# Optimization experiments

Measured on AMD Instinct MI355X. Metric: run time of the kernel, lower is better.

The kernel has to match this reference:

```python
import jax, jax.numpy as jnp
import numpy as np

INPUT_DIM = 1024
EMBED_DIM = 1024
NUM_HEADS = 16
HEAD_DIM = EMBED_DIM // NUM_HEADS


def _xavier_uniform(key, shape):
    fan_in, fan_out = shape[1], shape[0]
    limit = float(np.sqrt(6.0 / (fan_in + fan_out)))
    return jax.random.uniform(key, shape, jnp.float32, -limit, limit)


def setup_inputs() -> dict:
    key = jax.random.key(0)
    kx, kqkv, ko = jax.random.split(key, 3)
    x = jax.random.normal(kx, (2, 2048, INPUT_DIM), jnp.float32)
    # torch Linear stores weight as [out, in]; we keep that convention
    w_qkv = _xavier_uniform(kqkv, (3 * EMBED_DIM, INPUT_DIM))
    b_qkv = jnp.zeros((3 * EMBED_DIM,), jnp.float32)
    w_o = _xavier_uniform(ko, (EMBED_DIM, EMBED_DIM))
    b_o = jnp.zeros((EMBED_DIM,), jnp.float32)
    return {"x": x, "w_qkv": w_qkv, "b_qkv": b_qkv, "w_o": w_o, "b_o": b_o}


def reference(x, w_qkv, b_qkv, w_o, b_o):
    B, S, _ = x.shape
    H, D = NUM_HEADS, HEAD_DIM
    qkv = jnp.einsum("bsi,oi->bso", x, w_qkv) + b_qkv          # [B,S,3E]
    qkv = qkv.reshape(B, S, H, 3 * D).transpose(0, 2, 1, 3)    # [B,H,S,3D]
    q, k, v = jnp.split(qkv, 3, axis=-1)                        # each [B,H,S,D]
    scores = jnp.einsum("bhqd,bhkd->bhqk", q, k) / jnp.sqrt(jnp.float32(D))
    attn = jax.nn.softmax(scores, axis=-1)                      # [B,H,S,S]
    vals = jnp.einsum("bhqk,bhkd->bhqd", attn, v)               # [B,H,S,D]
    vals = vals.transpose(0, 2, 1, 3).reshape(B, S, H * D)      # [B,S,E]
    return jnp.einsum("bse,oe->bso", vals, w_o) + b_o
```

## Files before the change

### kernel.cpp

```cpp
#include <hip/hip_runtime.h>
#include <hip/hip_bf16.h>


typedef __attribute__((ext_vector_type(8))) short bf16x8;
typedef __attribute__((ext_vector_type(4))) short bf16x4;
typedef __attribute__((ext_vector_type(4))) float f32x4;

#define MFMA16(a, b, c) __builtin_amdgcn_mfma_f32_16x16x32_bf16((a), (b), (c), 0, 0, 0)

#if __has_builtin(__builtin_amdgcn_exp2f)
#define EXP2F(x) __builtin_amdgcn_exp2f(x)
#else
#define EXP2F(x) exp2f(x)
#endif

static __device__ __forceinline__ unsigned short f2bf_bits(float v) {
    __hip_bfloat16 h = __float2bfloat16(v);
    return *reinterpret_cast<unsigned short*>(&h);
}

static __device__ __forceinline__ bf16x8 cvt8(const float* p) {
    const f32x4 a = reinterpret_cast<const f32x4*>(p)[0];
    const f32x4 b = reinterpret_cast<const f32x4*>(p)[1];
    bf16x8 r;
    r[0] = (short)f2bf_bits(a[0]); r[1] = (short)f2bf_bits(a[1]);
    r[2] = (short)f2bf_bits(a[2]); r[3] = (short)f2bf_bits(a[3]);
    r[4] = (short)f2bf_bits(b[0]); r[5] = (short)f2bf_bits(b[1]);
    r[6] = (short)f2bf_bits(b[2]); r[7] = (short)f2bf_bits(b[3]);
    return r;
}

__device__ __forceinline__ bf16x8 ldg8(const __hip_bfloat16* p) {
    return *reinterpret_cast<const bf16x8*>(p);
}

__device__ __forceinline__ void load16_lds(const __hip_bfloat16* g, unsigned short* l) {
    __builtin_amdgcn_global_load_lds(
        (const __attribute__((address_space(1))) void*)g,
        (__attribute__((address_space(3))) void*)l, 16, 0, 0);
}

__global__ __launch_bounds__(256)
void cast2_f32_bf16(const float* __restrict__ x, __hip_bfloat16* __restrict__ xb,
                    const float* __restrict__ w, __hip_bfloat16* __restrict__ wb) {
    const int bid = blockIdx.x;
    const float* src = (bid < 512) ? x : w;
    __hip_bfloat16* dst = (bid < 512) ? xb : wb;
    const int rb = (bid < 512) ? bid : (bid - 512);
    const size_t base = (size_t)rb * 8192 + (size_t)threadIdx.x * 32;
#pragma unroll
    for (int i = 0; i < 4; ++i)
        *reinterpret_cast<bf16x8*>(dst + base + i * 8) = cvt8(src + base + i * 8);
}

__global__ __launch_bounds__(256)
void cast_f32_bf16(const float* __restrict__ src, __hip_bfloat16* __restrict__ dst) {
    const size_t base = ((size_t)blockIdx.x * 256 + threadIdx.x) * 32;
#pragma unroll
    for (int i = 0; i < 4; ++i)
        *reinterpret_cast<bf16x8*>(dst + base + i * 8) = cvt8(src + base + i * 8);
}

__global__ __launch_bounds__(256)
void qkv_gemm(const __hip_bfloat16* __restrict__ xb,
              const __hip_bfloat16* __restrict__ wb,
              const float* __restrict__ bqkv,
              __hip_bfloat16* __restrict__ Q,
              __hip_bfloat16* __restrict__ K,
              __hip_bfloat16* __restrict__ Vt) {
    __shared__ unsigned short As[2][128 * 32];
    __shared__ unsigned short Bs[2][128 * 32];

    const int tid  = threadIdx.x;
    const int lane = tid & 63;
    const int wv   = tid >> 6;
    const int quad = lane >> 4;
    const int l16  = lane & 15;
    const int wm   = wv >> 1;
    const int wn   = wv & 1;

    const int bid = blockIdx.x;
    const int xcd = bid & 7;
    const int r   = bid >> 3;
    const int m0  = (r / 3) * 128;
    const int n0  = (xcd * 3 + (r % 3)) * 128;

    const __hip_bfloat16* agl = xb + (size_t)(m0 + wv * 32 + (lane >> 2)) * 1024 + (lane & 3) * 8;
    const __hip_bfloat16* bgl = wb + (size_t)(n0 + wv * 32 + (lane >> 2)) * 1024 + (lane & 3) * 8;

    f32x4 zv = {0.f, 0.f, 0.f, 0.f};
    f32x4 acc[4][4];
#pragma unroll
    for (int ii = 0; ii < 4; ++ii)
#pragma unroll
        for (int jj = 0; jj < 4; ++jj) acc[ii][jj] = zv;

    load16_lds(agl, &As[0][(wv * 32) * 32]);
    load16_lds(agl + 16 * 1024, &As[0][(wv * 32 + 16) * 32]);
    load16_lds(bgl, &Bs[0][(wv * 32) * 32]);
    load16_lds(bgl + 16 * 1024, &Bs[0][(wv * 32 + 16) * 32]);
    __syncthreads();

    for (int k0 = 0; k0 < 1024; k0 += 32) {
        const int p = (k0 >> 5) & 1;
        if (k0 + 32 < 1024) {
            const int q = p ^ 1;
            load16_lds(agl + k0 + 32, &As[q][(wv * 32) * 32]);
            load16_lds(agl + 16 * 1024 + k0 + 32, &As[q][(wv * 32 + 16) * 32]);
            load16_lds(bgl + k0 + 32, &Bs[q][(wv * 32) * 32]);
            load16_lds(bgl + 16 * 1024 + k0 + 32, &Bs[q][(wv * 32 + 16) * 32]);
        }
        bf16x8 af[4], bf[4];
#pragma unroll
        for (int ii = 0; ii < 4; ++ii)
            af[ii] = *reinterpret_cast<const bf16x8*>(
                &As[p][(wm * 64 + ii * 16 + l16) * 32 + quad * 8]);
#pragma unroll
        for (int jj = 0; jj < 4; ++jj)
            bf[jj] = *reinterpret_cast<const bf16x8*>(
                &Bs[p][(wn * 64 + jj * 16 + l16) * 32 + quad * 8]);
#pragma unroll
        for (int ii = 0; ii < 4; ++ii)
#pragma unroll
            for (int jj = 0; jj < 4; ++jj)
                acc[ii][jj] = MFMA16(af[ii], bf[jj], acc[ii][jj]);
        __syncthreads();
    }

    const float QSCALE = 0.18033688011f;
    const int b  = m0 >> 11;
    const int s0 = m0 & 2047;

    const int nseg  = n0 + wn * 64;
    const int h     = nseg / 192;
    const int r2s   = nseg - h * 192;
    const int ttype = r2s >> 6;
    const int bh    = b * 16 + h;

    if (ttype == 2) {
#pragma unroll
        for (int jj = 0; jj < 4; ++jj) {
            const int d = jj * 16 + l16;
            const float bias = bqkv[nseg + d];
#pragma unroll
            for (int ii = 0; ii < 4; ++ii) {
                const int sk = s0 + wm * 64 + ii * 16 + quad * 4;
                bf16x4 pk;
#pragma unroll
                for (int i = 0; i < 4; ++i)
                    pk[i] = (short)f2bf_bits(acc[ii][jj][i] + bias);
                *reinterpret_cast<bf16x4*>(&Vt[((size_t)bh * 64 + d) * 2048 + sk]) = pk;
            }
        }
    } else {
        const float scl = (ttype == 0) ? QSCALE : 1.f;
        unsigned short* seg = (wn == 0) ? &As[0][0] : &Bs[0][0];
#pragma unroll
        for (int jj = 0; jj < 4; ++jj) {
            const int nl    = jj * 16 + l16;
            const float bias = bqkv[nseg + nl];
            const int cbase = nl >> 3;
            const int off   = nl & 7;
#pragma unroll
            for (int ii = 0; ii < 4; ++ii) {
#pragma unroll
                for (int i = 0; i < 4; ++i) {
                    const int m = wm * 64 + ii * 16 + quad * 4 + i;
                    const int c = cbase ^ (((m >> 2) & 3) << 1);
                    seg[m * 64 + c * 8 + off] =
                        f2bf_bits((acc[ii][jj][i] + bias) * scl);
                }
            }
        }
    }
    __syncthreads();

#pragma unroll
    for (int sgi = 0; sgi < 2; ++sgi) {
        const int nsg = n0 + sgi * 64;
        const int hh  = nsg / 192;
        const int rr  = nsg - hh * 192;
        const int tt  = rr >> 6;
        if (tt == 2) continue;
        __hip_bfloat16* gbase =
            ((tt == 0) ? Q : K) + ((size_t)(b * 16 + hh) * 2048 + s0) * 64;
        const unsigned short* seg = (sgi == 0) ? &As[0][0] : &Bs[0][0];
#pragma unroll
        for (int p4 = 0; p4 < 4; ++p4) {
            const int L = p4 * 256 + tid;
            const int m = L >> 3;
            const int c = (L & 7) ^ (((m >> 2) & 3) << 1);
            *reinterpret_cast<bf16x8*>(gbase + (size_t)L * 8) =
                *reinterpret_cast<const bf16x8*>(&seg[m * 64 + c * 8]);
        }
    }
}

__global__ __launch_bounds__(512, 4)
void attn_kernel(const __hip_bfloat16* __restrict__ Q,
                 const __hip_bfloat16* __restrict__ K,
                 const __hip_bfloat16* __restrict__ Vt,
                 __hip_bfloat16* __restrict__ AO) {
    __shared__ unsigned short SB[2][2][4096];
    __shared__ float LiX[4][2][64];

    const int tid  = threadIdx.x;
    const int lane = tid & 63;
    const int wv   = tid >> 6;
    const int grp  = wv >> 2;
    const int wq   = wv & 3;
    const int quad = lane >> 4;
    const int l16  = lane & 15;

    const int blk = blockIdx.x;
    const int xcd = blk & 7;
    const int sub = blk >> 3;
    const int bh  = xcd * 4 + (sub & 3);
    const int qb  = sub >> 2;
    const int q0  = qb * 128 + wq * 32;
    const int b   = bh >> 4;
    const int h   = bh & 15;
    const int key0 = grp * 1024;

    const __hip_bfloat16* Qp = Q  + (size_t)bh * 131072;
    const __hip_bfloat16* Kp = K  + (size_t)bh * 131072;
    const __hip_bfloat16* Vp = Vt + (size_t)bh * 131072;

    bf16x8 bQ[2][2];
#pragma unroll
    for (int t = 0; t < 2; ++t)
#pragma unroll
        for (int dh = 0; dh < 2; ++dh)
            bQ[t][dh] = ldg8(Qp + (size_t)(q0 + t * 16 + l16) * 64 + dh * 32 + quad * 8);

    const int keyg = (l16 >> 2) * 8 + (l16 & 3) + ((wq >> 1) << 2);
    const int kd0  = (wq & 1) * 32 + quad * 8;
    const __hip_bfloat16* ksrc = Kp + (size_t)(key0 + keyg) * 64 + kd0;
    const __hip_bfloat16* vsrc = Vp + (size_t)(wq * 16 + l16) * 2048 + key0 + quad * 8;

    const int gt = wq * 64 + lane;
    unsigned short* kd[2] = { &SB[grp][0][gt * 8],        &SB[grp][1][gt * 8] };
    unsigned short* vd[2] = { &SB[grp][0][gt * 8 + 2048], &SB[grp][1][gt * 8 + 2048] };

    f32x4 zv = {0.f, 0.f, 0.f, 0.f};
    f32x4 Of[2][4];
#pragma unroll
    for (int t = 0; t < 2; ++t)
#pragma unroll
        for (int jj = 0; jj < 4; ++jj) Of[t][jj] = zv;
    float li[2] = {0.f, 0.f};

    bf16x8 gk = ldg8(ksrc);
    bf16x8 gv = ldg8(vsrc);
    *reinterpret_cast<bf16x8*>(kd[0]) = gk;
    *reinterpret_cast<bf16x8*>(vd[0]) = gv;
    gk = ldg8(ksrc + 2048);
    gv = ldg8(vsrc + 32);
    __syncthreads();

    for (int kt = 0; kt < 32; ++kt) {
        const int p = kt & 1;
        if (kt < 31) {
            *reinterpret_cast<bf16x8*>(kd[p ^ 1]) = gk;
            *reinterpret_cast<bf16x8*>(vd[p ^ 1]) = gv;
        }
        if (kt < 30) {
            gk = ldg8(ksrc + (size_t)(kt + 2) * 2048);
            gv = ldg8(vsrc + (size_t)(kt + 2) * 32);
        }

        const unsigned short* base = &SB[grp][p][lane * 8];
        const bf16x8 aKA0 = *reinterpret_cast<const bf16x8*>(base + 0 * 512);
        const bf16x8 aKA1 = *reinterpret_cast<const bf16x8*>(base + 1 * 512);
        const bf16x8 aKB0 = *reinterpret_cast<const bf16x8*>(base + 2 * 512);
        const bf16x8 aKB1 = *reinterpret_cast<const bf16x8*>(base + 3 * 512);
        bf16x8 aV[4];
#pragma unroll
        for (int jj = 0; jj < 4; ++jj)
            aV[jj] = *reinterpret_cast<const bf16x8*>(base + (4 + jj) * 512);

        f32x4 sA[2], sB[2];
        __builtin_amdgcn_s_setprio(1);
#pragma unroll
        for (int t = 0; t < 2; ++t) {
            sA[t] = zv; sB[t] = zv;
            sA[t] = MFMA16(aKA0, bQ[t][0], sA[t]);
            sA[t] = MFMA16(aKA1, bQ[t][1], sA[t]);
            sB[t] = MFMA16(aKB0, bQ[t][0], sB[t]);
            sB[t] = MFMA16(aKB1, bQ[t][1], sB[t]);
        }
        __builtin_amdgcn_s_setprio(0);

#pragma unroll
        for (int t = 0; t < 2; ++t) {
            float pA[4], pB[4];
#pragma unroll
            for (int i = 0; i < 4; ++i) {
                pA[i] = EXP2F(sA[t][i]);
                pB[i] = EXP2F(sB[t][i]);
            }
            li[t] += ((pA[0] + pA[1]) + (pA[2] + pA[3]))
                   + ((pB[0] + pB[1]) + (pB[2] + pB[3]));

            bf16x8 bP;
            bP[0] = (short)f2bf_bits(pA[0]); bP[1] = (short)f2bf_bits(pA[1]);
            bP[2] = (short)f2bf_bits(pA[2]); bP[3] = (short)f2bf_bits(pA[3]);
            bP[4] = (short)f2bf_bits(pB[0]); bP[5] = (short)f2bf_bits(pB[1]);
            bP[6] = (short)f2bf_bits(pB[2]); bP[7] = (short)f2bf_bits(pB[3]);

            __builtin_amdgcn_s_setprio(1);
#pragma unroll
            for (int jj = 0; jj < 4; ++jj)
                Of[t][jj] = MFMA16(aV[jj], bP, Of[t][jj]);
            __builtin_amdgcn_s_setprio(0);
        }
        __syncthreads();
    }

#pragma unroll
    for (int t = 0; t < 2; ++t) {
        li[t] += __shfl_xor(li[t], 16);
        li[t] += __shfl_xor(li[t], 32);
    }

    f32x4* xf = reinterpret_cast<f32x4*>(&SB[0][0][0]);
    if (grp == 1) {
#pragma unroll
        for (int t = 0; t < 2; ++t) {
            LiX[wq][t][lane] = li[t];
#pragma unroll
            for (int jj = 0; jj < 4; ++jj)
                xf[wq * 512 + (t * 4 + jj) * 64 + lane] = Of[t][jj];
        }
    }
    __syncthreads();
    if (grp == 0) {
#pragma unroll
        for (int t = 0; t < 2; ++t) {
            const float linv = 1.f / (li[t] + LiX[wq][t][lane]);
            const int s = q0 + t * 16 + l16;
            __hip_bfloat16* aop = AO + (((size_t)b * 2048 + s) * 16 + h) * 64;
#pragma unroll
            for (int jj = 0; jj < 4; ++jj) {
                const f32x4 o2 = xf[wq * 512 + (t * 4 + jj) * 64 + lane];
                bf16x4 pk;
#pragma unroll
                for (int i = 0; i < 4; ++i)
                    pk[i] = (short)f2bf_bits((Of[t][jj][i] + o2[i]) * linv);
                *reinterpret_cast<bf16x4*>(aop + jj * 16 + quad * 4) = pk;
            }
        }
    }
}

__global__ __launch_bounds__(256)
void out_gemm(const __hip_bfloat16* __restrict__ A,
              const __hip_bfloat16* __restrict__ wob,
              const float* __restrict__ bo,
              float* __restrict__ out) {
    __shared__ unsigned short As[2][64 * 32];
    __shared__ unsigned short Bs[2][128 * 32];

    const int tid  = threadIdx.x;
    const int lane = tid & 63;
    const int wv   = tid >> 6;
    const int quad = lane >> 4;
    const int l16  = lane & 15;
    const int wm   = wv >> 1;
    const int wn   = wv & 1;

    const int bid = blockIdx.x;
    const int m0  = (bid >> 3) * 64;
    const int n0  = (bid & 7) * 128;

    const __hip_bfloat16* agl = A   + (size_t)(m0 + wv * 16 + (lane >> 2)) * 1024 + (lane & 3) * 8;
    const __hip_bfloat16* bgl = wob + (size_t)(n0 + wv * 32 + (lane >> 2)) * 1024 + (lane & 3) * 8;

    f32x4 zv = {0.f, 0.f, 0.f, 0.f};
    f32x4 acc[2][4];
#pragma unroll
    for (int ii = 0; ii < 2; ++ii)
#pragma unroll
        for (int jj = 0; jj < 4; ++jj) acc[ii][jj] = zv;

    load16_lds(agl, &As[0][(wv * 16) * 32]);
    load16_lds(bgl, &Bs[0][(wv * 32) * 32]);
    load16_lds(bgl + 16 * 1024, &Bs[0][(wv * 32 + 16) * 32]);
    __syncthreads();

    for (int k0 = 0; k0 < 1024; k0 += 32) {
        const int p = (k0 >> 5) & 1;
        if (k0 + 32 < 1024) {
            const int q = p ^ 1;
            load16_lds(agl + k0 + 32, &As[q][(wv * 16) * 32]);
            load16_lds(bgl + k0 + 32, &Bs[q][(wv * 32) * 32]);
            load16_lds(bgl + 16 * 1024 + k0 + 32, &Bs[q][(wv * 32 + 16) * 32]);
        }
        bf16x8 af[2], bf[4];
#pragma unroll
        for (int ii = 0; ii < 2; ++ii)
            af[ii] = *reinterpret_cast<const bf16x8*>(
                &As[p][(wm * 32 + ii * 16 + l16) * 32 + quad * 8]);
#pragma unroll
        for (int jj = 0; jj < 4; ++jj)
            bf[jj] = *reinterpret_cast<const bf16x8*>(
                &Bs[p][(wn * 64 + jj * 16 + l16) * 32 + quad * 8]);
#pragma unroll
        for (int ii = 0; ii < 2; ++ii)
#pragma unroll
            for (int jj = 0; jj < 4; ++jj)
                acc[ii][jj] = MFMA16(af[ii], bf[jj], acc[ii][jj]);
        __syncthreads();
    }

#pragma unroll
    for (int jj = 0; jj < 4; ++jj) {
        const int n = n0 + wn * 64 + jj * 16 + l16;
        const float bias = bo[n];
#pragma unroll
        for (int ii = 0; ii < 2; ++ii) {
#pragma unroll
            for (int i = 0; i < 4; ++i) {
                const int m = m0 + wm * 32 + ii * 16 + quad * 4 + i;
                out[(size_t)m * 1024 + n] = acc[ii][jj][i] + bias;
            }
        }
    }
}

extern "C" void kernel_launch(void* const* d_in, const int* in_sizes, int n_in,
                              void* d_out, int out_size, void* d_ws, size_t ws_size,
                              hipStream_t stream) {
    const float* x    = (const float*)d_in[0];
    const float* wqkv = (const float*)d_in[1];
    const float* bqkv = (const float*)d_in[2];
    const float* wo   = (const float*)d_in[3];
    const float* bo   = (const float*)d_in[4];
    float* out = (float*)d_out;

    __hip_bfloat16* ws = (__hip_bfloat16*)d_ws;
    __hip_bfloat16* Q   = ws;
    __hip_bfloat16* K   = ws + (size_t)4194304;
    __hip_bfloat16* Vt  = ws + (size_t)8388608;
    __hip_bfloat16* AO  = ws + (size_t)12582912;
    __hip_bfloat16* wob = Q;

    __hip_bfloat16* xb     = (__hip_bfloat16*)d_out;
    __hip_bfloat16* wqkvb  = xb + (size_t)4194304;

    cast2_f32_bf16<<<dim3(896), 256, 0, stream>>>(x, xb, wqkv, wqkvb);
    qkv_gemm<<<dim3(768), 256, 0, stream>>>(xb, wqkvb, bqkv, Q, K, Vt);
    attn_kernel<<<dim3(512), 512, 0, stream>>>(Q, K, Vt, AO);
    cast_f32_bf16<<<dim3(128), 256, 0, stream>>>(wo, wob);
    out_gemm<<<dim3(512), 256, 0, stream>>>(AO, wob, bo, out);
}
```

Measured before the change: 190.1 us.

## Split attention keys across two blocks with atomic fp32 accumulation and combine pass

Doubles the attention grid by splitting the 2048 keys into two halves handled by separate blocks, so 1024 blocks run instead of 512. Each block atomically adds its unnormalized output and row sums into fp32 buffers zeroed by a new kernel. A combine kernel then normalizes and casts to bf16, and it also absorbs the w_o cast. The aim is better GPU occupancy in the attention stage. In exchange it adds global fp32 atomics, an extra zeroing kernel, and more memory traffic.

```diff
diff --git a/kernel.cpp b/kernel.cpp
--- a/kernel.cpp
+++ b/kernel.cpp
@@ -54,11 +54,14 @@
 }
 
 __global__ __launch_bounds__(256)
-void cast_f32_bf16(const float* __restrict__ src, __hip_bfloat16* __restrict__ dst) {
-    const size_t base = ((size_t)blockIdx.x * 256 + threadIdx.x) * 32;
-#pragma unroll
-    for (int i = 0; i < 4; ++i)
-        *reinterpret_cast<bf16x8*>(dst + base + i * 8) = cvt8(src + base + i * 8);
+void zero_f32(float* __restrict__ aof, float* __restrict__ li) {
+    const int bid = blockIdx.x;
+    float* dst = (bid < 1024) ? (aof + (size_t)bid * 4096)
+                              : (li + (size_t)(bid - 1024) * 4096);
+    const f32x4 z = {0.f, 0.f, 0.f, 0.f};
+    f32x4* p = reinterpret_cast<f32x4*>(dst + (size_t)threadIdx.x * 16);
+#pragma unroll
+    for (int i = 0; i < 4; ++i) p[i] = z;
 }
 
 __global__ __launch_bounds__(256)
@@ -200,7 +203,8 @@
 void attn_kernel(const __hip_bfloat16* __restrict__ Q,
                  const __hip_bfloat16* __restrict__ K,
                  const __hip_bfloat16* __restrict__ Vt,
-                 __hip_bfloat16* __restrict__ AO) {
+                 float* __restrict__ AOf,
+                 float* __restrict__ LI) {
     __shared__ unsigned short SB[2][2][4096];
     __shared__ float LiX[4][2][64];
 
@@ -216,11 +220,12 @@
     const int xcd = blk & 7;
     const int sub = blk >> 3;
     const int bh  = xcd * 4 + (sub & 3);
-    const int qb  = sub >> 2;
+    const int qb  = (sub >> 2) & 15;
+    const int ks  = sub >> 6;
     const int q0  = qb * 128 + wq * 32;
     const int b   = bh >> 4;
     const int h   = bh & 15;
-    const int key0 = grp * 1024;
+    const int key0 = ks * 1024 + grp * 512;
 
     const __hip_bfloat16* Qp = Q  + (size_t)bh * 131072;
     const __hip_bfloat16* Kp = K  + (size_t)bh * 131072;
@@ -258,13 +263,13 @@
     gv = ldg8(vsrc + 32);
     __syncthreads();
 
-    for (int kt = 0; kt < 32; ++kt) {
+    for (int kt = 0; kt < 16; ++kt) {
         const int p = kt & 1;
-        if (kt < 31) {
+        if (kt < 15) {
             *reinterpret_cast<bf16x8*>(kd[p ^ 1]) = gk;
             *reinterpret_cast<bf16x8*>(vd[p ^ 1]) = gv;
         }
-        if (kt < 30) {
+        if (kt < 14) {
             gk = ldg8(ksrc + (size_t)(kt + 2) * 2048);
             gv = ldg8(vsrc + (size_t)(kt + 2) * 32);
         }
@@ -337,19 +342,47 @@
     if (grp == 0) {
 #pragma unroll
         for (int t = 0; t < 2; ++t) {
-            const float linv = 1.f / (li[t] + LiX[wq][t][lane]);
+            const float lsum = li[t] + LiX[wq][t][lane];
             const int s = q0 + t * 16 + l16;
-            __hip_bfloat16* aop = AO + (((size_t)b * 2048 + s) * 16 + h) * 64;
+            if (quad == 0)
+                atomicAdd(&LI[(size_t)bh * 2048 + s], lsum);
+            float* aop = AOf + (((size_t)b * 2048 + s) * 16 + h) * 64;
 #pragma unroll
             for (int jj = 0; jj < 4; ++jj) {
                 const f32x4 o2 = xf[wq * 512 + (t * 4 + jj) * 64 + lane];
-                bf16x4 pk;
 #pragma unroll
                 for (int i = 0; i < 4; ++i)
-                    pk[i] = (short)f2bf_bits((Of[t][jj][i] + o2[i]) * linv);
-                *reinterpret_cast<bf16x4*>(aop + jj * 16 + quad * 4) = pk;
+                    atomicAdd(&aop[jj * 16 + quad * 4 + i], Of[t][jj][i] + o2[i]);
             }
         }
+    }
+}
+
+__global__ __launch_bounds__(256)
+void combine_cast(const float* __restrict__ AOf, const float* __restrict__ LI,
+                  __hip_bfloat16* __restrict__ AO,
+                  const float* __restrict__ wo, __hip_bfloat16* __restrict__ wob) {
+    const int bid = blockIdx.x;
+    if (bid < 2048) {
+        const size_t g = (size_t)bid * 2048 + (size_t)threadIdx.x * 8;
+        const int b = (int)(g >> 21);
+        const int s = (int)(g >> 10) & 2047;
+        const int h = (int)(g >> 6) & 15;
+        const float linv = 1.f / LI[((size_t)b * 16 + h) * 2048 + s];
+        const f32x4 a0 = *reinterpret_cast<const f32x4*>(AOf + g);
+        const f32x4 a1 = *reinterpret_cast<const f32x4*>(AOf + g + 4);
+        bf16x8 r;
+        r[0] = (short)f2bf_bits(a0[0] * linv); r[1] = (short)f2bf_bits(a0[1] * linv);
+        r[2] = (short)f2bf_bits(a0[2] * linv); r[3] = (short)f2bf_bits(a0[3] * linv);
+        r[4] = (short)f2bf_bits(a1[0] * linv); r[5] = (short)f2bf_bits(a1[1] * linv);
+        r[6] = (short)f2bf_bits(a1[2] * linv); r[7] = (short)f2bf_bits(a1[3] * linv);
+        *reinterpret_cast<bf16x8*>(AO + g) = r;
+    } else {
+        const int rb = bid - 2048;
+        const size_t base = (size_t)rb * 8192 + (size_t)threadIdx.x * 32;
+#pragma unroll
+        for (int i = 0; i < 4; ++i)
+            *reinterpret_cast<bf16x8*>(wob + base + i * 8) = cvt8(wo + base + i * 8);
     }
 }
 
@@ -442,15 +475,18 @@
     __hip_bfloat16* Q   = ws;
     __hip_bfloat16* K   = ws + (size_t)4194304;
     __hip_bfloat16* Vt  = ws + (size_t)8388608;
-    __hip_bfloat16* AO  = ws + (size_t)12582912;
-    __hip_bfloat16* wob = Q;
+    float*          LI  = (float*)(ws + (size_t)12582912);
+    __hip_bfloat16* AO  = Q;
+    __hip_bfloat16* wob = K;
 
     __hip_bfloat16* xb     = (__hip_bfloat16*)d_out;
     __hip_bfloat16* wqkvb  = xb + (size_t)4194304;
+    float*          AOf    = (float*)d_out;
 
     cast2_f32_bf16<<<dim3(896), 256, 0, stream>>>(x, xb, wqkv, wqkvb);
     qkv_gemm<<<dim3(768), 256, 0, stream>>>(xb, wqkvb, bqkv, Q, K, Vt);
-    attn_kernel<<<dim3(512), 512, 0, stream>>>(Q, K, Vt, AO);
-    cast_f32_bf16<<<dim3(128), 256, 0, stream>>>(wo, wob);
+    zero_f32<<<dim3(1040), 256, 0, stream>>>(AOf, LI);
+    attn_kernel<<<dim3(1024), 512, 0, stream>>>(Q, K, Vt, AOf, LI);
+    combine_cast<<<dim3(2176), 256, 0, stream>>>(AOf, LI, AO, wo, wob);
     out_gemm<<<dim3(512), 256, 0, stream>>>(AO, wob, bo, out);
 }
```

Measured after the change: 282.5 us. +48.6%, slower.
